# Kernel tuning notes

Measured on AMD Instinct MI355X. Metric: run time of the kernel, lower is better.

The kernel has to match this reference:

```python
import jax, jax.numpy as jnp
import numpy as np

B, T = 32, 512
IN, D, H, HD, L, FFN = 375, 512, 8, 64, 6, 1024
NC, CD, LAT, K = 4, 64, 256, 512
DL, DH, DFF, OUT = 4, 512, 1024, 291


def setup_inputs() -> dict:
    key = jax.random.key(0)
    ks = iter(jax.random.split(key, 64))
    def p(shape, scale=0.02):
        return jax.random.normal(next(ks), shape, jnp.float32) * scale
    return {
        "x": jax.random.normal(next(ks), (B, T, IN), jnp.float32),
        "in_w": p((IN, D)), "in_b": jnp.zeros((D,), jnp.float32),
        "enc_ln1_s": jnp.ones((L, D), jnp.float32), "enc_ln1_b": jnp.zeros((L, D), jnp.float32),
        "enc_qkv_w": p((L, D, 3 * D)), "enc_qkv_b": jnp.zeros((L, 3 * D), jnp.float32),
        "enc_out_w": p((L, D, D)), "enc_out_b": jnp.zeros((L, D), jnp.float32),
        "enc_ln2_s": jnp.ones((L, D), jnp.float32), "enc_ln2_b": jnp.zeros((L, D), jnp.float32),
        "enc_ff1_w": p((L, D, FFN)), "enc_ff1_b": jnp.zeros((L, FFN), jnp.float32),
        "enc_ff2_w": p((L, FFN, D)), "enc_ff2_b": jnp.zeros((L, D), jnp.float32),
        "lat_w": p((D, LAT)), "lat_b": jnp.zeros((LAT,), jnp.float32),
        "codebook": jax.random.uniform(next(ks), (K, CD), jnp.float32, -1.0 / K, 1.0 / K),
        "unlat_w": p((LAT, DH)), "unlat_b": jnp.zeros((DH,), jnp.float32),
        "dec_ln_s": jnp.ones((DL, DH), jnp.float32), "dec_ln_b": jnp.zeros((DL, DH), jnp.float32),
        "dec_ff1_w": p((DL, DH, DFF)), "dec_ff1_b": jnp.zeros((DL, DFF), jnp.float32),
        "dec_ff2_w": p((DL, DFF, DH)), "dec_ff2_b": jnp.zeros((DL, DH), jnp.float32),
        "out_w": p((DH, OUT)), "out_b": jnp.zeros((OUT,), jnp.float32),
    }


def _ln(x, s, b):
    m = x.mean(-1, keepdims=True)
    v = jnp.var(x, axis=-1, keepdims=True)
    return (x - m) / jnp.sqrt(v + 1e-5) * s + b


def _rope(x, cos, sin):
    # interleaved even/odd rotation, matches torch stack(...,-1).flatten(-2)
    xe, xo = x[..., 0::2], x[..., 1::2]
    re = xe * cos - xo * sin
    ro = xe * sin + xo * cos
    return jnp.stack((re, ro), axis=-1).reshape(x.shape)


def _forward(x, in_w, in_b, enc_ln1_s, enc_ln1_b, enc_qkv_w, enc_qkv_b,
             enc_out_w, enc_out_b, enc_ln2_s, enc_ln2_b, enc_ff1_w, enc_ff1_b,
             enc_ff2_w, enc_ff2_b, lat_w, lat_b, codebook, unlat_w, unlat_b,
             dec_ln_s, dec_ln_b, dec_ff1_w, dec_ff1_b, dec_ff2_w, dec_ff2_b,
             out_w, out_b):
    h = x @ in_w + in_b  # [B,T,D]
    inv_freq = 1.0 / (10000.0 ** (jnp.arange(0, HD, 2, dtype=jnp.float32) / HD))
    freqs = jnp.outer(jnp.arange(T, dtype=jnp.float32), inv_freq)  # [T, HD/2]
    cos, sin = jnp.cos(freqs), jnp.sin(freqs)
    for i in range(L):
        y = _ln(h, enc_ln1_s[i], enc_ln1_b[i])
        qkv = (y @ enc_qkv_w[i] + enc_qkv_b[i]).reshape(B, T, 3, H, HD)
        qkv = qkv.transpose(2, 0, 3, 1, 4)  # [3,B,H,T,HD]
        q, k, v = qkv[0], qkv[1], qkv[2]
        q = _rope(q, cos, sin)
        k = _rope(k, cos, sin)
        sc = jnp.einsum('bhqd,bhkd->bhqk', q, k) / np.float32(np.sqrt(HD))
        probs = jax.nn.softmax(sc, axis=-1)
        a = jnp.einsum('bhqk,bhkd->bhqd', probs, v)
        a = a.transpose(0, 2, 1, 3).reshape(B, T, D)
        h = h + (a @ enc_out_w[i] + enc_out_b[i])
        y = _ln(h, enc_ln2_s[i], enc_ln2_b[i])
        h = h + (jax.nn.gelu(y @ enc_ff1_w[i] + enc_ff1_b[i], approximate=False)
                 @ enc_ff2_w[i] + enc_ff2_b[i])
    # VQ bottleneck: split each token latent into NC subvectors, nearest code each
    z_bt = (h @ lat_w + lat_b).reshape(B * T, LAT)
    flat_z = z_bt.reshape(-1, CD)  # [B*T*NC, CD]
    d = ((flat_z ** 2).sum(1, keepdims=True)
         - 2.0 * (flat_z @ codebook.T)
         + (codebook ** 2).sum(1))  # [B*T*NC, K]
    idx = jnp.argmin(d, axis=1)
    q_bt = codebook[idx].reshape(B * T, LAT)
    st = z_bt + jax.lax.stop_gradient(q_bt - z_bt)  # straight-through
    g = st.reshape(B, T, LAT) @ unlat_w + unlat_b
    for i in range(DL):
        y = _ln(g, dec_ln_s[i], dec_ln_b[i])
        g = g + (jax.nn.gelu(y @ dec_ff1_w[i] + dec_ff1_b[i], approximate=False)
                 @ dec_ff2_w[i] + dec_ff2_b[i])
    return g @ out_w + out_b  # [B,T,291]


def reference(x, in_w, in_b, enc_ln1_s, enc_ln1_b, enc_qkv_w, enc_qkv_b,
              enc_out_w, enc_out_b, enc_ln2_s, enc_ln2_b, enc_ff1_w, enc_ff1_b,
              enc_ff2_w, enc_ff2_b, lat_w, lat_b, codebook, unlat_w, unlat_b,
              dec_ln_s, dec_ln_b, dec_ff1_w, dec_ff1_b, dec_ff2_w, dec_ff2_b,
              out_w, out_b):
    return _forward(x, in_w, in_b, enc_ln1_s, enc_ln1_b, enc_qkv_w, enc_qkv_b,
                    enc_out_w, enc_out_b, enc_ln2_s, enc_ln2_b, enc_ff1_w, enc_ff1_b,
                    enc_ff2_w, enc_ff2_b, lat_w, lat_b, codebook, unlat_w, unlat_b,
                    dec_ln_s, dec_ln_b, dec_ff1_w, dec_ff1_b, dec_ff2_w, dec_ff2_b,
                    out_w, out_b)
```

## Files before the change

kernel.cpp:

```cpp
#include <hip/hip_runtime.h>
#include <hip/hip_bf16.h>

#define BB 32
#define TT 512
#define IND 375
#define DD 512
#define HH 8
#define HDD 64
#define LL 6
#define FFNN 1024
#define LATD 256
#define KCODES 512
#define DLL 4
#define DHH 512
#define DFFF 1024
#define OUTD 291
#define MTOK (BB*TT)

__global__ void rope_table_k(float* __restrict__ cosb, float* __restrict__ sinb) {
  int idx = blockIdx.x * blockDim.x + threadIdx.x;
  if (idx >= TT * 32) return;
  int t = idx >> 5, i = idx & 31;
  float inv = powf(10000.0f, -(float)(2 * i) / 64.0f);
  float f = (float)t * inv;
  cosb[idx] = cosf(f);
  sinb[idx] = sinf(f);
}

template<int EPI>
__global__ __launch_bounds__(256) void gemm128_k(const float* __restrict__ A,
                                                 const float* __restrict__ W,
                                                 const float* __restrict__ bias,
                                                 const float* __restrict__ R,
                                                 float* __restrict__ C,
                                                 int M, int K, int N,
                                                 const float* __restrict__ COS,
                                                 const float* __restrict__ SIN) {
  __shared__ float As[16][128];
  __shared__ float4 Bs4[16][2][16];
  const int bn = blockIdx.x * 128;
  const int bm = blockIdx.y * 128;
  const int tid = threadIdx.x;
  const int tx = tid & 15;
  const int ty = tid >> 4;
  const int ar = tid >> 1;
  const int ak = (tid & 1) * 8;
  const int bk = tid >> 4;
  const int bx = tid & 15;

  float acc[8][8] = {};

  for (int k0 = 0; k0 < K; k0 += 16) {
    const float* ap = A + (size_t)(bm + ar) * K + k0 + ak;
    float4 a0 = *(const float4*)ap;
    float4 a1 = *(const float4*)(ap + 4);
    const float* bp = W + (size_t)(k0 + bk) * N + bn + bx * 8;
    float4 b0 = *(const float4*)bp;
    float4 b1 = *(const float4*)(bp + 4);

    __syncthreads();
    As[ak + 0][ar] = a0.x; As[ak + 1][ar] = a0.y; As[ak + 2][ar] = a0.z; As[ak + 3][ar] = a0.w;
    As[ak + 4][ar] = a1.x; As[ak + 5][ar] = a1.y; As[ak + 6][ar] = a1.z; As[ak + 7][ar] = a1.w;
    Bs4[bk][0][bx] = b0;
    Bs4[bk][1][bx] = b1;
    __syncthreads();

#pragma unroll
    for (int kk = 0; kk < 16; ++kk) {
      float4 va0 = *(const float4*)&As[kk][ty * 8];
      float4 va1 = *(const float4*)&As[kk][ty * 8 + 4];
      float4 vb0 = Bs4[kk][0][tx];
      float4 vb1 = Bs4[kk][1][tx];
      float av[8] = {va0.x, va0.y, va0.z, va0.w, va1.x, va1.y, va1.z, va1.w};
      float bv[8] = {vb0.x, vb0.y, vb0.z, vb0.w, vb1.x, vb1.y, vb1.z, vb1.w};
#pragma unroll
      for (int ii = 0; ii < 8; ++ii)
#pragma unroll
        for (int jj = 0; jj < 8; ++jj)
          acc[ii][jj] = __builtin_fmaf(av[ii], bv[jj], acc[ii][jj]);
    }
  }

#pragma unroll
  for (int ii = 0; ii < 8; ++ii) {
    int m = bm + ty * 8 + ii;
#pragma unroll
    for (int g = 0; g < 2; ++g) {
      int n0 = bn + tx * 8 + g * 4;
      float t4[4];
#pragma unroll
      for (int j = 0; j < 4; ++j) {
        float v = acc[ii][g * 4 + j] + bias[n0 + j];
        if (EPI == 1) v += R[(size_t)m * N + n0 + j];
        if (EPI == 2) v = 0.5f * v * (1.0f + erff(v * 0.70710678118654752f));
        t4[j] = v;
      }
      if (EPI == 3 && n0 < 2 * DD) {
        int tpos = m & 511;
        int i0 = (n0 & 63) >> 1;
        float c0 = COS[tpos * 32 + i0],     s0 = SIN[tpos * 32 + i0];
        float c1 = COS[tpos * 32 + i0 + 1], s1 = SIN[tpos * 32 + i0 + 1];
        float xe0 = t4[0], xo0 = t4[1], xe1 = t4[2], xo1 = t4[3];
        t4[0] = xe0 * c0 - xo0 * s0;
        t4[1] = xe0 * s0 + xo0 * c0;
        t4[2] = xe1 * c1 - xo1 * s1;
        t4[3] = xe1 * s1 + xo1 * c1;
      }
      float4 vv; vv.x = t4[0]; vv.y = t4[1]; vv.z = t4[2]; vv.w = t4[3];
      *(float4*)&C[(size_t)m * N + n0] = vv;
    }
  }
}

template<int EPI>
__global__ __launch_bounds__(256) void gemm128g_k(const float* __restrict__ A,
                                                  const float* __restrict__ W,
                                                  const float* __restrict__ bias,
                                                  const float* __restrict__ R,
                                                  float* __restrict__ C,
                                                  int M, int K, int N) {
  __shared__ float As[16][128];
  __shared__ float4 Bs4[16][2][16];
  const int bn = blockIdx.x * 128;
  const int bm = blockIdx.y * 128;
  const int tid = threadIdx.x;
  const int tx = tid & 15, ty = tid >> 4;
  float acc[8][8] = {};
  float* Bsf = (float*)Bs4;

  const int nt = (K + 15) >> 4;
  for (int t = 0; t < nt; ++t) {
    const int k0 = t * 16;
    __syncthreads();
#pragma unroll
    for (int i = 0; i < 8; ++i) {
      int e = tid + i * 256;
      int r = e & 127, kk = e >> 7;
      int kg = k0 + kk;
      As[kk][r] = (kg < K) ? A[(size_t)(bm + r) * K + kg] : 0.0f;
    }
#pragma unroll
    for (int i = 0; i < 8; ++i) {
      int e = tid + i * 256;
      int n = e & 127, kk = e >> 7;
      int kg = k0 + kk, ng = bn + n;
      float w = (kg < K && ng < N) ? W[(size_t)kg * N + ng] : 0.0f;
      Bsf[kk * 128 + ((n >> 2) & 1) * 64 + (n >> 3) * 4 + (n & 3)] = w;
    }
    __syncthreads();
#pragma unroll
    for (int kk = 0; kk < 16; ++kk) {
      float4 va0 = *(const float4*)&As[kk][ty * 8];
      float4 va1 = *(const float4*)&As[kk][ty * 8 + 4];
      float4 vb0 = Bs4[kk][0][tx];
      float4 vb1 = Bs4[kk][1][tx];
      float av[8] = {va0.x, va0.y, va0.z, va0.w, va1.x, va1.y, va1.z, va1.w};
      float bv[8] = {vb0.x, vb0.y, vb0.z, vb0.w, vb1.x, vb1.y, vb1.z, vb1.w};
#pragma unroll
      for (int ii = 0; ii < 8; ++ii)
#pragma unroll
        for (int jj = 0; jj < 8; ++jj)
          acc[ii][jj] = __builtin_fmaf(av[ii], bv[jj], acc[ii][jj]);
    }
  }

#pragma unroll
  for (int ii = 0; ii < 8; ++ii) {
    int m = bm + ty * 8 + ii;
#pragma unroll
    for (int jj = 0; jj < 8; ++jj) {
      int n = bn + tx * 8 + jj;
      if (n >= N) continue;
      float v = acc[ii][jj] + bias[n];
      if (EPI == 1) v += R[(size_t)m * N + n];
      if (EPI == 2) v = 0.5f * v * (1.0f + erff(v * 0.70710678118654752f));
      C[(size_t)m * N + n] = v;
    }
  }
}

__global__ __launch_bounds__(256) void ln_k(const float* __restrict__ X,
                                            const float* __restrict__ s,
                                            const float* __restrict__ b,
                                            float* __restrict__ Y) {
  int wave = threadIdx.x >> 6, lane = threadIdx.x & 63;
  int row = blockIdx.x * 4 + wave;
  const float* x = X + (size_t)row * DD;
  float v[8];
  float sum = 0.0f;
#pragma unroll
  for (int j = 0; j < 8; ++j) { v[j] = x[lane + 64 * j]; sum += v[j]; }
#pragma unroll
  for (int o = 32; o; o >>= 1) sum += __shfl_xor(sum, o);
  float mean = sum * (1.0f / 512.0f);
  float var = 0.0f;
#pragma unroll
  for (int j = 0; j < 8; ++j) { float d = v[j] - mean; var += d * d; }
#pragma unroll
  for (int o = 32; o; o >>= 1) var += __shfl_xor(var, o);
  float inv = 1.0f / sqrtf(var * (1.0f / 512.0f) + 1e-5f);
  float* y = Y + (size_t)row * DD;
#pragma unroll
  for (int j = 0; j < 8; ++j) {
    int d = lane + 64 * j;
    y[d] = (v[j] - mean) * inv * s[d] + b[d];
  }
}

__global__ __launch_bounds__(256) void fattn_k(const float* __restrict__ qkv,
                                               float* __restrict__ out) {
  __shared__ float Qs[64][68];
  __shared__ float KVs[64][68];
  __shared__ float Ps[64][68];
  const int tid = threadIdx.x;
  const int tx = tid & 15, ty = tid >> 4;
  const int g = blockIdx.x;
  const int xcd = g & 7, slot = g >> 3;
  const int qt = slot & 7;
  const int p = ((slot >> 3) << 3) | xcd;
  const int h = p & 7;
  const int b = p >> 3;
  const float* base = qkv + (size_t)b * TT * (3 * DD) + h * HDD;

  {
    int r = tid & 63, q0 = tid >> 6;
#pragma unroll
    for (int jj = 0; jj < 4; ++jj) {
      int q = q0 + jj * 4;
      float4 v = *(const float4*)(base + (size_t)(qt * 64 + r) * (3 * DD) + q * 4);
      Qs[q * 4 + 0][r] = v.x; Qs[q * 4 + 1][r] = v.y;
      Qs[q * 4 + 2][r] = v.z; Qs[q * 4 + 3][r] = v.w;
    }
  }

  float o[4][4] = {};
  float m[4] = {-1e30f, -1e30f, -1e30f, -1e30f};
  float l[4] = {0.f, 0.f, 0.f, 0.f};

  for (int kt = 0; kt < 8; ++kt) {
    __syncthreads();
    {
      int r = tid & 63, q0 = tid >> 6;
#pragma unroll
      for (int jj = 0; jj < 4; ++jj) {
        int q = q0 + jj * 4;
        float4 v = *(const float4*)(base + (size_t)(kt * 64 + r) * (3 * DD) + DD + q * 4);
        KVs[q * 4 + 0][r] = v.x; KVs[q * 4 + 1][r] = v.y;
        KVs[q * 4 + 2][r] = v.z; KVs[q * 4 + 3][r] = v.w;
      }
    }
    __syncthreads();

    float s[4][4] = {};
#pragma unroll 4
    for (int d = 0; d < 64; ++d) {
      float4 a4 = *(const float4*)&Qs[d][ty * 4];
      float4 b4 = *(const float4*)&KVs[d][tx * 4];
      float av[4] = {a4.x, a4.y, a4.z, a4.w};
      float bv[4] = {b4.x, b4.y, b4.z, b4.w};
#pragma unroll
      for (int ii = 0; ii < 4; ++ii)
#pragma unroll
        for (int jj = 0; jj < 4; ++jj)
          s[ii][jj] = __builtin_fmaf(av[ii], bv[jj], s[ii][jj]);
    }

#pragma unroll
    for (int i = 0; i < 4; ++i) {
      float mm = fmaxf(fmaxf(s[i][0], s[i][1]), fmaxf(s[i][2], s[i][3])) * 0.125f;
#pragma unroll
      for (int off = 1; off < 16; off <<= 1) mm = fmaxf(mm, __shfl_xor(mm, off));
      float mn = fmaxf(m[i], mm);
      float f = expf(m[i] - mn);
      m[i] = mn;
      float ls = 0.0f;
#pragma unroll
      for (int j = 0; j < 4; ++j) {
        float pp = expf(__builtin_fmaf(s[i][j], 0.125f, -mn));
        s[i][j] = pp;
        ls += pp;
      }
#pragma unroll
      for (int off = 1; off < 16; off <<= 1) ls += __shfl_xor(ls, off);
      l[i] = __builtin_fmaf(l[i], f, ls);
#pragma unroll
      for (int j = 0; j < 4; ++j) o[i][j] *= f;
    }

    __syncthreads();

#pragma unroll
    for (int j = 0; j < 4; ++j) {
      float4 pv; pv.x = s[0][j]; pv.y = s[1][j]; pv.z = s[2][j]; pv.w = s[3][j];
      *(float4*)&Ps[tx * 4 + j][ty * 4] = pv;
    }
#pragma unroll
    for (int ii = 0; ii < 4; ++ii) {
      int e = tid + 256 * ii;
      int c = e >> 4, q = e & 15;
      float4 v = *(const float4*)(base + (size_t)(kt * 64 + c) * (3 * DD) + 2 * DD + q * 4);
      *(float4*)&KVs[c][q * 4] = v;
    }
    __syncthreads();

#pragma unroll 4
    for (int c = 0; c < 64; ++c) {
      float4 a4 = *(const float4*)&Ps[c][ty * 4];
      float4 b4 = *(const float4*)&KVs[c][tx * 4];
      float av[4] = {a4.x, a4.y, a4.z, a4.w};
      float bv[4] = {b4.x, b4.y, b4.z, b4.w};
#pragma unroll
      for (int ii = 0; ii < 4; ++ii)
#pragma unroll
        for (int jj = 0; jj < 4; ++jj)
          o[ii][jj] = __builtin_fmaf(av[ii], bv[jj], o[ii][jj]);
    }
  }

#pragma unroll
  for (int i = 0; i < 4; ++i) {
    float inv = 1.0f / l[i];
    int tok = b * TT + qt * 64 + ty * 4 + i;
    float4 vv;
    vv.x = o[i][0] * inv; vv.y = o[i][1] * inv;
    vv.z = o[i][2] * inv; vv.w = o[i][3] * inv;
    *(float4*)&out[(size_t)tok * DD + h * HDD + tx * 4] = vv;
  }
}

__device__ __forceinline__ float npsumsq64(const float* __restrict__ a) {
  float r0 = __fmul_rn(a[0], a[0]), r1 = __fmul_rn(a[1], a[1]);
  float r2 = __fmul_rn(a[2], a[2]), r3 = __fmul_rn(a[3], a[3]);
  float r4 = __fmul_rn(a[4], a[4]), r5 = __fmul_rn(a[5], a[5]);
  float r6 = __fmul_rn(a[6], a[6]), r7 = __fmul_rn(a[7], a[7]);
#pragma unroll
  for (int i = 8; i < 64; i += 8) {
    r0 = __fadd_rn(r0, __fmul_rn(a[i + 0], a[i + 0]));
    r1 = __fadd_rn(r1, __fmul_rn(a[i + 1], a[i + 1]));
    r2 = __fadd_rn(r2, __fmul_rn(a[i + 2], a[i + 2]));
    r3 = __fadd_rn(r3, __fmul_rn(a[i + 3], a[i + 3]));
    r4 = __fadd_rn(r4, __fmul_rn(a[i + 4], a[i + 4]));
    r5 = __fadd_rn(r5, __fmul_rn(a[i + 5], a[i + 5]));
    r6 = __fadd_rn(r6, __fmul_rn(a[i + 6], a[i + 6]));
    r7 = __fadd_rn(r7, __fmul_rn(a[i + 7], a[i + 7]));
  }
  return __fadd_rn(__fadd_rn(__fadd_rn(r0, r1), __fadd_rn(r2, r3)),
                   __fadd_rn(__fadd_rn(r4, r5), __fadd_rn(r6, r7)));
}

__global__ void vqs2_k(const float* __restrict__ CB, float* __restrict__ S2) {
  int k = blockIdx.x * 256 + threadIdx.x;
  if (k < KCODES) S2[k] = npsumsq64(CB + (size_t)k * 64);
}

__global__ __launch_bounds__(256) void vq32b_k(const float* __restrict__ Z,
                                               const float* __restrict__ CB,
                                               const float* __restrict__ S2,
                                               int* __restrict__ idxOut) {
  __shared__ float zs[16][68];
  __shared__ float cs[64][68];
  __shared__ float s2s[64];
  __shared__ float rv[256];
  __shared__ int   ri[256];
  const int tid = threadIdx.x;
  const int lr = tid >> 4;
  const int sub = tid & 15;
  const int row0 = blockIdx.x * 16;

  {
    int r = tid >> 4, q = tid & 15;
    *(float4*)&zs[r][q * 4] = *(const float4*)(Z + (size_t)(row0 + r) * 64 + q * 4);
  }
  __syncthreads();

  const float S1 = npsumsq64(zs[lr]);

  float bv = 3.4e38f;
  int bi = 0x7fffffff;
  for (int ct = 0; ct < 8; ++ct) {
    __syncthreads();
    for (int e = tid; e < 1024; e += 256) {
      int r = e >> 4, q = e & 15;
      *(float4*)&cs[r][q * 4] = *(const float4*)(CB + (size_t)(ct * 64 + r) * 64 + q * 4);
    }
    if (tid < 64) s2s[tid] = S2[ct * 64 + tid];
    __syncthreads();
#pragma unroll
    for (int cc = 0; cc < 4; ++cc) {
      int kl = cc * 16 + sub;
      float g = 0.0f;
#pragma unroll
      for (int d4 = 0; d4 < 16; ++d4) {
        float4 zf = *(const float4*)&zs[lr][d4 * 4];
        float4 cf = *(const float4*)&cs[kl][d4 * 4];
        g = __builtin_fmaf(zf.x, cf.x, g);
        g = __builtin_fmaf(zf.y, cf.y, g);
        g = __builtin_fmaf(zf.z, cf.z, g);
        g = __builtin_fmaf(zf.w, cf.w, g);
      }
      float d32 = __fadd_rn(__fsub_rn(S1, __fmul_rn(2.0f, g)), s2s[kl]);
      int k = ct * 64 + kl;
      if (d32 < bv || (d32 == bv && k < bi)) { bv = d32; bi = k; }
    }
  }
  rv[tid] = bv; ri[tid] = bi;
  __syncthreads();
  if (sub == 0) {
    float bb = rv[tid]; int ii = ri[tid];
#pragma unroll
    for (int j = 1; j < 16; ++j) {
      float v = rv[tid + j]; int id = ri[tid + j];
      if (v < bb || (v == bb && id < ii)) { bb = v; ii = id; }
    }
    idxOut[row0 + lr] = ii;
  }
}

__global__ void stgather_k(const float* __restrict__ Z, const float* __restrict__ CB,
                           const int* __restrict__ idx, float* __restrict__ Q) {
  int e = blockIdx.x * blockDim.x + threadIdx.x;
  if (e >= MTOK * LATD) return;
  int chunk = e >> 6, d = e & 63;
  int k = idx[chunk] & (KCODES - 1);
  float z = Z[e];
  float c = CB[(size_t)k * 64 + d];
  Q[e] = __fadd_rn(z, __fsub_rn(c, z));
}

static inline dim3 g128(int M, int N) { return dim3(N / 128, M / 128); }

extern "C" void kernel_launch(void* const* d_in, const int* in_sizes, int n_in,
                              void* d_out, int out_size, void* d_ws, size_t ws_size,
                              hipStream_t stream) {
  const float* x        = (const float*)d_in[0];
  const float* in_w     = (const float*)d_in[1];
  const float* in_b     = (const float*)d_in[2];
  const float* ln1_s    = (const float*)d_in[3];
  const float* ln1_b    = (const float*)d_in[4];
  const float* qkv_w    = (const float*)d_in[5];
  const float* qkv_b    = (const float*)d_in[6];
  const float* aout_w   = (const float*)d_in[7];
  const float* aout_b   = (const float*)d_in[8];
  const float* ln2_s    = (const float*)d_in[9];
  const float* ln2_b    = (const float*)d_in[10];
  const float* ff1_w    = (const float*)d_in[11];
  const float* ff1_b    = (const float*)d_in[12];
  const float* ff2_w    = (const float*)d_in[13];
  const float* ff2_b    = (const float*)d_in[14];
  const float* lat_w    = (const float*)d_in[15];
  const float* lat_b    = (const float*)d_in[16];
  const float* codebook = (const float*)d_in[17];
  const float* unlat_w  = (const float*)d_in[18];
  const float* unlat_b  = (const float*)d_in[19];
  const float* dln_s    = (const float*)d_in[20];
  const float* dln_b    = (const float*)d_in[21];
  const float* dff1_w   = (const float*)d_in[22];
  const float* dff1_b   = (const float*)d_in[23];
  const float* dff2_w   = (const float*)d_in[24];
  const float* dff2_b   = (const float*)d_in[25];
  const float* ow       = (const float*)d_in[26];
  const float* ob       = (const float*)d_in[27];
  float* out = (float*)d_out;

  float* ws   = (float*)d_ws;
  float* Hb   = ws;
  float* Yb   = Hb + (size_t)MTOK * DD;
  float* QKVb = Yb + (size_t)MTOK * DD;
  float* COSb = QKVb + (size_t)MTOK * 3 * DD;
  float* SINb = COSb + TT * 32;
  int*   IDXb = (int*)(SINb + TT * 32);
  float* S2b  = (float*)(IDXb + MTOK * 4);

  dim3 blk(256);

  rope_table_k<<<(TT * 32 + 255) / 256, blk, 0, stream>>>(COSb, SINb);
  vqs2_k<<<2, blk, 0, stream>>>(codebook, S2b);

  gemm128g_k<0><<<dim3(4, 128), blk, 0, stream>>>(x, in_w, in_b, nullptr, Hb, MTOK, IND, DD);

  for (int l = 0; l < LL; ++l) {
    ln_k<<<MTOK / 4, blk, 0, stream>>>(Hb, ln1_s + l * DD, ln1_b + l * DD, Yb);
    gemm128_k<3><<<g128(MTOK, 3 * DD), blk, 0, stream>>>(Yb, qkv_w + (size_t)l * DD * 3 * DD,
                                                         qkv_b + l * 3 * DD, nullptr, QKVb,
                                                         MTOK, DD, 3 * DD, COSb, SINb);
    fattn_k<<<BB * HH * (TT / 64), blk, 0, stream>>>(QKVb, Yb);
    gemm128_k<1><<<g128(MTOK, DD), blk, 0, stream>>>(Yb, aout_w + (size_t)l * DD * DD,
                                                     aout_b + l * DD, Hb, Hb, MTOK, DD, DD,
                                                     nullptr, nullptr);
    ln_k<<<MTOK / 4, blk, 0, stream>>>(Hb, ln2_s + l * DD, ln2_b + l * DD, Yb);
    gemm128_k<2><<<g128(MTOK, FFNN), blk, 0, stream>>>(Yb, ff1_w + (size_t)l * DD * FFNN,
                                                       ff1_b + l * FFNN, nullptr, QKVb,
                                                       MTOK, DD, FFNN, nullptr, nullptr);
    gemm128_k<1><<<g128(MTOK, DD), blk, 0, stream>>>(QKVb, ff2_w + (size_t)l * FFNN * DD,
                                                     ff2_b + l * DD, Hb, Hb, MTOK, FFNN, DD,
                                                     nullptr, nullptr);
  }

  gemm128_k<0><<<g128(MTOK, LATD), blk, 0, stream>>>(Hb, lat_w, lat_b, nullptr, Yb,
                                                     MTOK, DD, LATD, nullptr, nullptr);
  vq32b_k<<<(MTOK * 4) / 16, blk, 0, stream>>>(Yb, codebook, S2b, IDXb);
  stgather_k<<<(MTOK * LATD) / 256, blk, 0, stream>>>(Yb, codebook, IDXb, QKVb);
  gemm128_k<0><<<g128(MTOK, DHH), blk, 0, stream>>>(QKVb, unlat_w, unlat_b, nullptr, Hb,
                                                    MTOK, LATD, DHH, nullptr, nullptr);

  for (int l = 0; l < DLL; ++l) {
    ln_k<<<MTOK / 4, blk, 0, stream>>>(Hb, dln_s + l * DHH, dln_b + l * DHH, Yb);
    gemm128_k<2><<<g128(MTOK, DFFF), blk, 0, stream>>>(Yb, dff1_w + (size_t)l * DHH * DFFF,
                                                       dff1_b + l * DFFF, nullptr, QKVb,
                                                       MTOK, DHH, DFFF, nullptr, nullptr);
    gemm128_k<1><<<g128(MTOK, DHH), blk, 0, stream>>>(QKVb, dff2_w + (size_t)l * DFFF * DHH,
                                                      dff2_b + l * DHH, Hb, Hb, MTOK, DFFF, DHH,
                                                      nullptr, nullptr);
  }

  gemm128g_k<0><<<dim3(3, 128), blk, 0, stream>>>(Hb, ow, ob, nullptr, out, MTOK, DHH, OUTD);
}
```

Measured before the change: 9.582 ms.

## Double GEMM K-tile to 32 and pad ragged GEMMs onto the vectorized kernel

The main fp32 GEMM now stages a 32-deep K slice per iteration instead of 16, halving the number of barrier pairs per output tile at the cost of twice the shared memory. The scalar-load guarded GEMM used for the input projection (K=375) and output projection (N=291) is removed. Those two GEMMs now go through the vectorized kernel on zero-padded copies of the input, the weights and the output buffer, with extra pad and unpad kernels that cost additional memory traffic.

```diff
diff --git a/kernel.cpp b/kernel.cpp
--- a/kernel.cpp
+++ b/kernel.cpp
@@ -16,6 +16,8 @@
 #define DFFF 1024
 #define OUTD 291
 #define MTOK (BB*TT)
+#define KPAD 384
+#define NPAD 384
 
 __global__ void rope_table_k(float* __restrict__ cosb, float* __restrict__ sinb) {
   int idx = blockIdx.x * blockDim.x + threadIdx.x;
@@ -25,6 +27,35 @@
   float f = (float)t * inv;
   cosb[idx] = cosf(f);
   sinb[idx] = sinf(f);
+}
+
+__global__ void pad_x_k(const float* __restrict__ x, float* __restrict__ Xp) {
+  int m = blockIdx.x;
+  const float* src = x + (size_t)m * IND;
+  float* dst = Xp + (size_t)m * KPAD;
+  for (int k = threadIdx.x; k < KPAD; k += 256)
+    dst[k] = (k < IND) ? src[k] : 0.0f;
+}
+__global__ void pad_wx_k(const float* __restrict__ w, float* __restrict__ Wp) {
+  int e = blockIdx.x * 256 + threadIdx.x;
+  if (e >= KPAD * DD) return;
+  int k = e >> 9, n = e & 511;
+  Wp[e] = (k < IND) ? w[(size_t)k * DD + n] : 0.0f;
+}
+__global__ void pad_wo_k(const float* __restrict__ w, const float* __restrict__ b,
+                         float* __restrict__ Wp, float* __restrict__ bp) {
+  int e = blockIdx.x * 256 + threadIdx.x;
+  if (e >= DHH * NPAD) return;
+  int k = e / NPAD, n = e - k * NPAD;
+  Wp[e] = (n < OUTD) ? w[(size_t)k * OUTD + n] : 0.0f;
+  if (e < NPAD) bp[e] = (e < OUTD) ? b[e] : 0.0f;
+}
+__global__ void unpad_k(const float* __restrict__ Cp, float* __restrict__ out) {
+  int m = blockIdx.x;
+  const float* src = Cp + (size_t)m * NPAD;
+  float* dst = out + (size_t)m * OUTD;
+  for (int n = threadIdx.x; n < OUTD; n += 256)
+    dst[n] = src[n];
 }
 
 template<int EPI>
@@ -36,37 +67,45 @@
                                                  int M, int K, int N,
                                                  const float* __restrict__ COS,
                                                  const float* __restrict__ SIN) {
-  __shared__ float As[16][128];
-  __shared__ float4 Bs4[16][2][16];
+  __shared__ float As[32][128];
+  __shared__ float4 Bs4[32][2][16];
   const int bn = blockIdx.x * 128;
   const int bm = blockIdx.y * 128;
   const int tid = threadIdx.x;
   const int tx = tid & 15;
   const int ty = tid >> 4;
   const int ar = tid >> 1;
-  const int ak = (tid & 1) * 8;
-  const int bk = tid >> 4;
-  const int bx = tid & 15;
+  const int ak = (tid & 1) * 16;
+  const int bk = tid >> 3;
+  const int bxs = tid & 7;
 
   float acc[8][8] = {};
 
-  for (int k0 = 0; k0 < K; k0 += 16) {
+  for (int k0 = 0; k0 < K; k0 += 32) {
     const float* ap = A + (size_t)(bm + ar) * K + k0 + ak;
     float4 a0 = *(const float4*)ap;
     float4 a1 = *(const float4*)(ap + 4);
-    const float* bp = W + (size_t)(k0 + bk) * N + bn + bx * 8;
+    float4 a2 = *(const float4*)(ap + 8);
+    float4 a3 = *(const float4*)(ap + 12);
+    const float* bp = W + (size_t)(k0 + bk) * N + bn + bxs * 16;
     float4 b0 = *(const float4*)bp;
     float4 b1 = *(const float4*)(bp + 4);
-
-    __syncthreads();
-    As[ak + 0][ar] = a0.x; As[ak + 1][ar] = a0.y; As[ak + 2][ar] = a0.z; As[ak + 3][ar] = a0.w;
-    As[ak + 4][ar] = a1.x; As[ak + 5][ar] = a1.y; As[ak + 6][ar] = a1.z; As[ak + 7][ar] = a1.w;
-    Bs4[bk][0][bx] = b0;
-    Bs4[bk][1][bx] = b1;
-    __syncthreads();
-
-#pragma unroll
-    for (int kk = 0; kk < 16; ++kk) {
+    float4 b2 = *(const float4*)(bp + 8);
+    float4 b3 = *(const float4*)(bp + 12);
+
+    __syncthreads();
+    As[ak +  0][ar] = a0.x; As[ak +  1][ar] = a0.y; As[ak +  2][ar] = a0.z; As[ak +  3][ar] = a0.w;
+    As[ak +  4][ar] = a1.x; As[ak +  5][ar] = a1.y; As[ak +  6][ar] = a1.z; As[ak +  7][ar] = a1.w;
+    As[ak +  8][ar] = a2.x; As[ak +  9][ar] = a2.y; As[ak + 10][ar] = a2.z; As[ak + 11][ar] = a2.w;
+    As[ak + 12][ar] = a3.x; As[ak + 13][ar] = a3.y; As[ak + 14][ar] = a3.z; As[ak + 15][ar] = a3.w;
+    Bs4[bk][0][2 * bxs]     = b0;
+    Bs4[bk][1][2 * bxs]     = b1;
+    Bs4[bk][0][2 * bxs + 1] = b2;
+    Bs4[bk][1][2 * bxs + 1] = b3;
+    __syncthreads();
+
+#pragma unroll
+    for (int kk = 0; kk < 32; ++kk) {
       float4 va0 = *(const float4*)&As[kk][ty * 8];
       float4 va1 = *(const float4*)&As[kk][ty * 8 + 4];
       float4 vb0 = Bs4[kk][0][tx];
@@ -108,73 +147,6 @@
       }
       float4 vv; vv.x = t4[0]; vv.y = t4[1]; vv.z = t4[2]; vv.w = t4[3];
       *(float4*)&C[(size_t)m * N + n0] = vv;
-    }
-  }
-}
-
-template<int EPI>
-__global__ __launch_bounds__(256) void gemm128g_k(const float* __restrict__ A,
-                                                  const float* __restrict__ W,
-                                                  const float* __restrict__ bias,
-                                                  const float* __restrict__ R,
-                                                  float* __restrict__ C,
-                                                  int M, int K, int N) {
-  __shared__ float As[16][128];
-  __shared__ float4 Bs4[16][2][16];
-  const int bn = blockIdx.x * 128;
-  const int bm = blockIdx.y * 128;
-  const int tid = threadIdx.x;
-  const int tx = tid & 15, ty = tid >> 4;
-  float acc[8][8] = {};
-  float* Bsf = (float*)Bs4;
-
-  const int nt = (K + 15) >> 4;
-  for (int t = 0; t < nt; ++t) {
-    const int k0 = t * 16;
-    __syncthreads();
-#pragma unroll
-    for (int i = 0; i < 8; ++i) {
-      int e = tid + i * 256;
-      int r = e & 127, kk = e >> 7;
-      int kg = k0 + kk;
-      As[kk][r] = (kg < K) ? A[(size_t)(bm + r) * K + kg] : 0.0f;
-    }
-#pragma unroll
-    for (int i = 0; i < 8; ++i) {
-      int e = tid + i * 256;
-      int n = e & 127, kk = e >> 7;
-      int kg = k0 + kk, ng = bn + n;
-      float w = (kg < K && ng < N) ? W[(size_t)kg * N + ng] : 0.0f;
-      Bsf[kk * 128 + ((n >> 2) & 1) * 64 + (n >> 3) * 4 + (n & 3)] = w;
-    }
-    __syncthreads();
-#pragma unroll
-    for (int kk = 0; kk < 16; ++kk) {
-      float4 va0 = *(const float4*)&As[kk][ty * 8];
-      float4 va1 = *(const float4*)&As[kk][ty * 8 + 4];
-      float4 vb0 = Bs4[kk][0][tx];
-      float4 vb1 = Bs4[kk][1][tx];
-      float av[8] = {va0.x, va0.y, va0.z, va0.w, va1.x, va1.y, va1.z, va1.w};
-      float bv[8] = {vb0.x, vb0.y, vb0.z, vb0.w, vb1.x, vb1.y, vb1.z, vb1.w};
-#pragma unroll
-      for (int ii = 0; ii < 8; ++ii)
-#pragma unroll
-        for (int jj = 0; jj < 8; ++jj)
-          acc[ii][jj] = __builtin_fmaf(av[ii], bv[jj], acc[ii][jj]);
-    }
-  }
-
-#pragma unroll
-  for (int ii = 0; ii < 8; ++ii) {
-    int m = bm + ty * 8 + ii;
-#pragma unroll
-    for (int jj = 0; jj < 8; ++jj) {
-      int n = bn + tx * 8 + jj;
-      if (n >= N) continue;
-      float v = acc[ii][jj] + bias[n];
-      if (EPI == 1) v += R[(size_t)m * N + n];
-      if (EPI == 2) v = 0.5f * v * (1.0f + erff(v * 0.70710678118654752f));
-      C[(size_t)m * N + n] = v;
     }
   }
 }
@@ -470,13 +442,22 @@
   float* SINb = COSb + TT * 32;
   int*   IDXb = (int*)(SINb + TT * 32);
   float* S2b  = (float*)(IDXb + MTOK * 4);
+  float* WXp  = S2b + KCODES;
+  float* WOp  = WXp + (size_t)KPAD * DD;
+  float* BOp  = WOp + (size_t)DHH * NPAD;
+  float* Xp   = QKVb;
+  float* Cp   = QKVb;
 
   dim3 blk(256);
 
   rope_table_k<<<(TT * 32 + 255) / 256, blk, 0, stream>>>(COSb, SINb);
   vqs2_k<<<2, blk, 0, stream>>>(codebook, S2b);
-
-  gemm128g_k<0><<<dim3(4, 128), blk, 0, stream>>>(x, in_w, in_b, nullptr, Hb, MTOK, IND, DD);
+  pad_wx_k<<<(KPAD * DD + 255) / 256, blk, 0, stream>>>(in_w, WXp);
+  pad_wo_k<<<(DHH * NPAD + 255) / 256, blk, 0, stream>>>(ow, ob, WOp, BOp);
+  pad_x_k<<<MTOK, blk, 0, stream>>>(x, Xp);
+
+  gemm128_k<0><<<g128(MTOK, DD), blk, 0, stream>>>(Xp, WXp, in_b, nullptr, Hb,
+                                                   MTOK, KPAD, DD, nullptr, nullptr);
 
   for (int l = 0; l < LL; ++l) {
     ln_k<<<MTOK / 4, blk, 0, stream>>>(Hb, ln1_s + l * DD, ln1_b + l * DD, Yb);
@@ -513,5 +494,7 @@
                                                       nullptr, nullptr);
   }
 
-  gemm128g_k<0><<<dim3(3, 128), blk, 0, stream>>>(Hb, ow, ob, nullptr, out, MTOK, DHH, OUTD);
-}
+  gemm128_k<0><<<g128(MTOK, NPAD), blk, 0, stream>>>(Hb, WOp, BOp, nullptr, Cp,
+                                                     MTOK, DHH, NPAD, nullptr, nullptr);
+  unpad_k<<<MTOK, blk, 0, stream>>>(Cp, out);
+}
```

Result: faster. 8.868 ms (-7.5%).
